# Kernel tuning notes

Measured on AMD Instinct MI355X. Metric: run time of the kernel, lower is better.

Reference implementation:

```python
import jax, jax.numpy as jnp
import numpy as np

N = 50000
IN_C, HID_C, CLS_C = 512, 256, 128
E = 800000


def setup_inputs() -> dict:
    key = jax.random.key(0)
    k1, k2, k3, k4, k5, k6 = jax.random.split(key, 6)
    x = jax.random.normal(k1, (N, IN_C), dtype=jnp.float32)
    edge_index = jax.random.randint(k2, (2, E), 0, N, dtype=jnp.int64)
    # GCNConv params (glorot weights, zero bias as in PyG init)
    W1 = jax.random.normal(k3, (IN_C, HID_C), dtype=jnp.float32) * (1.0 / np.sqrt(IN_C))
    b1 = jnp.zeros((HID_C,), dtype=jnp.float32)
    W2 = jax.random.normal(k4, (HID_C, CLS_C), dtype=jnp.float32) * (1.0 / np.sqrt(HID_C))
    b2 = jnp.zeros((CLS_C,), dtype=jnp.float32)
    return {"x": x, "W1": W1, "b1": b1, "W2": W2, "b2": b2, "edge_index": edge_index}


def _norm_edges(edge_index, n):
    # PyG GCNConv: add self-loops, symmetric normalization deg^-1/2
    loops = jnp.arange(n, dtype=edge_index.dtype)
    src = jnp.concatenate([edge_index[0], loops])
    dst = jnp.concatenate([edge_index[1], loops])
    ones = jnp.ones_like(src, dtype=jnp.float32)
    deg = jax.ops.segment_sum(ones, dst, num_segments=n)
    dinv = jnp.where(deg > 0, jax.lax.rsqrt(deg), 0.0)
    norm = dinv[src] * dinv[dst]  # [E+N]
    return src, dst, norm


def _gcn_conv(x, W, b, src, dst, norm, n):
    h = x @ W  # project first (out_channels < in_channels)
    msg = h[src] * norm[:, None]  # gather + scale, [E+N, C]
    out = jax.ops.segment_sum(msg, dst, num_segments=n)  # scatter-add
    return out + b


def reference(x, W1, b1, W2, b2, edge_index):
    n = x.shape[0]
    src, dst, norm = _norm_edges(edge_index, n)
    h = jax.nn.relu(_gcn_conv(x, W1, b1, src, dst, norm, n))
    # dropout p=0.5 is a no-op in eval mode
    out = _gcn_conv(h, W2, b2, src, dst, norm, n)
    return jax.nn.sigmoid(out)
```

## Files before the change

kernel.cpp:

```cpp
#include <hip/hip_runtime.h>

typedef __attribute__((ext_vector_type(8))) short bf16x8;
typedef __attribute__((ext_vector_type(4))) float f32x4;
typedef unsigned short u16;

__device__ __forceinline__ float bf2f(u16 u) {
  union { unsigned int i; float f; } c; c.i = ((unsigned int)u) << 16; return c.f;
}
__device__ __forceinline__ u16 f2bf(float f) {
  union { float f; unsigned int i; } c; c.f = f;
  unsigned int u = c.i;
  unsigned int r = (u + 0x7FFFu + ((u >> 16) & 1u)) >> 16;
  return (u16)r;
}


__global__ void k_init_deg(int* deg, int n) {
  int i = blockIdx.x * 256 + threadIdx.x;
  if (i < n) deg[i] = 1;
}

__global__ void k_count(const int* __restrict__ ei, int* deg, int E) {
  int e = blockIdx.x * 256 + threadIdx.x;
  if (e < E) atomicAdd(&deg[ei[E + e]], 1);
}

__global__ void k_blocksum(const int* __restrict__ deg, int* bsum, int n) {
  __shared__ int s[256];
  int t = threadIdx.x;
  int i = blockIdx.x * 256 + t;
  s[t] = (i < n) ? (deg[i] - 1) : 0;
  __syncthreads();
  for (int o = 128; o > 0; o >>= 1) {
    if (t < o) s[t] += s[t + o];
    __syncthreads();
  }
  if (t == 0) bsum[blockIdx.x] = s[0];
}

__global__ void k_scanb(const int* __restrict__ bsum, int* bofs, int nb) {
  __shared__ int s[256];
  int t = threadIdx.x;
  int v = (t < nb) ? bsum[t] : 0;
  s[t] = v;
  __syncthreads();
  for (int o = 1; o < 256; o <<= 1) {
    int x = (t >= o) ? s[t - o] : 0;
    __syncthreads();
    s[t] += x;
    __syncthreads();
  }
  bofs[t] = s[t] - v;
}

__global__ void k_rowptr(const int* __restrict__ deg, const int* __restrict__ bofs,
                         int* rowptr, int* cursor, float* dinv, int n) {
  __shared__ int s[256];
  int t = threadIdx.x;
  int i = blockIdx.x * 256 + t;
  int d = (i < n) ? deg[i] : 1;
  int v = (i < n) ? (d - 1) : 0;
  s[t] = v;
  __syncthreads();
  for (int o = 1; o < 256; o <<= 1) {
    int x = (t >= o) ? s[t - o] : 0;
    __syncthreads();
    s[t] += x;
    __syncthreads();
  }
  int excl = s[t] - v + bofs[blockIdx.x];
  if (i < n) {
    rowptr[i] = excl;
    cursor[i] = excl;
    dinv[i] = rsqrtf((float)d);
    if (i == n - 1) rowptr[n] = excl + v;
  }
}

__global__ void k_fill(const int* __restrict__ ei, int* cursor, int* col, int E) {
  int e = blockIdx.x * 256 + threadIdx.x;
  if (e >= E) return;
  int s = ei[e];
  int d = ei[E + e];
  int pos = atomicAdd(&cursor[d], 1);
  col[pos] = s;
}

__global__ void k_twt(const float* __restrict__ W, u16* __restrict__ Wt, int K, int N) {
  int i = blockIdx.x * 256 + threadIdx.x;
  if (i >= K * N) return;
  int k = i / N, n = i - k * N;
  Wt[n * K + k] = f2bf(W[i]);
}


template <bool AF32, int K>
__launch_bounds__(256)
__global__ void gemm_kernel(const void* __restrict__ Ap, const u16* __restrict__ Bt,
                            u16* __restrict__ C, int M, int ldc) {
  __shared__ u16 As[128][40];
  __shared__ u16 Bs[128][40];
  const int tid = threadIdx.x;
  const int lane = tid & 63;
  const int wid = tid >> 6;
  const int wr = wid >> 1, wc = wid & 1;
  const long brow = (long)blockIdx.x * 128;
  const long bcol = (long)blockIdx.y * 128;
  const int srow = tid >> 1;
  const int kb = (tid & 1) << 4;

  f32x4 acc[4][4];
#pragma unroll
  for (int i = 0; i < 4; i++)
#pragma unroll
    for (int j = 0; j < 4; j++) acc[i][j] = (f32x4){0.f, 0.f, 0.f, 0.f};

  union Pack { u16 s[16]; uint4 v[2]; };
  Pack pa, pb;
  constexpr int NT = K / 32;

  auto stage = [&](int kt) {
    const long rgA = brow + srow;
    if constexpr (AF32) {
      const float* A = (const float*)Ap;
      if (rgA < M) {
        const float4* p = (const float4*)(A + rgA * (long)K + kt * 32 + kb);
#pragma unroll
        for (int i = 0; i < 4; i++) {
          float4 v = p[i];
          pa.s[4 * i + 0] = f2bf(v.x);
          pa.s[4 * i + 1] = f2bf(v.y);
          pa.s[4 * i + 2] = f2bf(v.z);
          pa.s[4 * i + 3] = f2bf(v.w);
        }
      } else {
#pragma unroll
        for (int i = 0; i < 16; i++) pa.s[i] = 0;
      }
    } else {
      const u16* A = (const u16*)Ap;
      const uint4* p = (const uint4*)(A + rgA * (long)K + kt * 32 + kb);
      pa.v[0] = p[0];
      pa.v[1] = p[1];
    }
    const uint4* q = (const uint4*)(Bt + (bcol + srow) * (long)K + kt * 32 + kb);
    pb.v[0] = q[0];
    pb.v[1] = q[1];
  };

  stage(0);
  for (int kt = 0; kt < NT; ++kt) {
    __syncthreads();
    *(uint4*)&As[srow][kb] = pa.v[0];
    *(uint4*)&As[srow][kb + 8] = pa.v[1];
    *(uint4*)&Bs[srow][kb] = pb.v[0];
    *(uint4*)&Bs[srow][kb + 8] = pb.v[1];
    __syncthreads();
    if (kt + 1 < NT) stage(kt + 1);

    bf16x8 af[4], bf[4];
#pragma unroll
    for (int i = 0; i < 4; i++)
      af[i] = *(const bf16x8*)&As[wr * 64 + i * 16 + (lane & 15)][(lane >> 4) * 8];
#pragma unroll
    for (int j = 0; j < 4; j++)
      bf[j] = *(const bf16x8*)&Bs[wc * 64 + j * 16 + (lane & 15)][(lane >> 4) * 8];
#pragma unroll
    for (int i = 0; i < 4; i++)
#pragma unroll
      for (int j = 0; j < 4; j++)
        acc[i][j] = __builtin_amdgcn_mfma_f32_16x16x32_bf16(af[i], bf[j], acc[i][j], 0, 0, 0);
  }

#pragma unroll
  for (int i = 0; i < 4; i++) {
    const long r0 = brow + wr * 64 + i * 16 + ((lane >> 4) * 4);
#pragma unroll
    for (int j = 0; j < 4; j++) {
      const long cc = bcol + wc * 64 + j * 16 + (lane & 15);
#pragma unroll
      for (int q = 0; q < 4; q++) {
        long r = r0 + q;
        if (r < M) C[r * (long)ldc + cc] = f2bf(acc[i][j][q]);
      }
    }
  }
}


__launch_bounds__(256)
__global__ void agg1(const u16* __restrict__ h0, const int* __restrict__ rowptr,
                     const int* __restrict__ col, const float* __restrict__ dinv,
                     const float* __restrict__ b1, u16* __restrict__ h, int n) {
  const int wid = threadIdx.x >> 6, lane = threadIdx.x & 63;
  const int node = blockIdx.x * 4 + wid;
  if (node >= n) return;
  const float di = dinv[node];
  ushort4 sv = ((const ushort4*)(h0 + (size_t)node * 256))[lane];
  float a0 = di * bf2f(sv.x), a1 = di * bf2f(sv.y), a2 = di * bf2f(sv.z), a3 = di * bf2f(sv.w);
  int e = rowptr[node];
  const int r1 = rowptr[node + 1];
  for (; e + 4 <= r1; e += 4) {
    int s0 = col[e], s1 = col[e + 1], s2 = col[e + 2], s3 = col[e + 3];
    float c0 = dinv[s0], c1 = dinv[s1], c2 = dinv[s2], c3 = dinv[s3];
    ushort4 v0 = ((const ushort4*)(h0 + (size_t)s0 * 256))[lane];
    ushort4 v1 = ((const ushort4*)(h0 + (size_t)s1 * 256))[lane];
    ushort4 v2 = ((const ushort4*)(h0 + (size_t)s2 * 256))[lane];
    ushort4 v3 = ((const ushort4*)(h0 + (size_t)s3 * 256))[lane];
    a0 += c0 * bf2f(v0.x) + c1 * bf2f(v1.x) + c2 * bf2f(v2.x) + c3 * bf2f(v3.x);
    a1 += c0 * bf2f(v0.y) + c1 * bf2f(v1.y) + c2 * bf2f(v2.y) + c3 * bf2f(v3.y);
    a2 += c0 * bf2f(v0.z) + c1 * bf2f(v1.z) + c2 * bf2f(v2.z) + c3 * bf2f(v3.z);
    a3 += c0 * bf2f(v0.w) + c1 * bf2f(v1.w) + c2 * bf2f(v2.w) + c3 * bf2f(v3.w);
  }
  for (; e < r1; ++e) {
    int s = col[e];
    float c = dinv[s];
    ushort4 v = ((const ushort4*)(h0 + (size_t)s * 256))[lane];
    a0 += c * bf2f(v.x); a1 += c * bf2f(v.y); a2 += c * bf2f(v.z); a3 += c * bf2f(v.w);
  }
  float4 bb = ((const float4*)b1)[lane];
  a0 = a0 * di + bb.x; a1 = a1 * di + bb.y; a2 = a2 * di + bb.z; a3 = a3 * di + bb.w;
  a0 = a0 > 0.f ? a0 : 0.f; a1 = a1 > 0.f ? a1 : 0.f;
  a2 = a2 > 0.f ? a2 : 0.f; a3 = a3 > 0.f ? a3 : 0.f;
  ushort4 o; o.x = f2bf(a0); o.y = f2bf(a1); o.z = f2bf(a2); o.w = f2bf(a3);
  ((ushort4*)(h + (size_t)node * 256))[lane] = o;
}

__device__ __forceinline__ float sigmoidf_(float x) { return 1.f / (1.f + __expf(-x)); }

__launch_bounds__(256)
__global__ void agg2(const u16* __restrict__ h2, const int* __restrict__ rowptr,
                     const int* __restrict__ col, const float* __restrict__ dinv,
                     const float* __restrict__ b2, float* __restrict__ out, int n) {
  const int wid = threadIdx.x >> 6, lane = threadIdx.x & 63;
  const int node = blockIdx.x * 4 + wid;
  if (node >= n) return;
  const float di = dinv[node];
  ushort2 sv = ((const ushort2*)(h2 + (size_t)node * 128))[lane];
  float a0 = di * bf2f(sv.x), a1 = di * bf2f(sv.y);
  int e = rowptr[node];
  const int r1 = rowptr[node + 1];
  for (; e + 4 <= r1; e += 4) {
    int s0 = col[e], s1 = col[e + 1], s2 = col[e + 2], s3 = col[e + 3];
    float c0 = dinv[s0], c1 = dinv[s1], c2 = dinv[s2], c3 = dinv[s3];
    ushort2 v0 = ((const ushort2*)(h2 + (size_t)s0 * 128))[lane];
    ushort2 v1 = ((const ushort2*)(h2 + (size_t)s1 * 128))[lane];
    ushort2 v2 = ((const ushort2*)(h2 + (size_t)s2 * 128))[lane];
    ushort2 v3 = ((const ushort2*)(h2 + (size_t)s3 * 128))[lane];
    a0 += c0 * bf2f(v0.x) + c1 * bf2f(v1.x) + c2 * bf2f(v2.x) + c3 * bf2f(v3.x);
    a1 += c0 * bf2f(v0.y) + c1 * bf2f(v1.y) + c2 * bf2f(v2.y) + c3 * bf2f(v3.y);
  }
  for (; e < r1; ++e) {
    int s = col[e];
    float c = dinv[s];
    ushort2 v = ((const ushort2*)(h2 + (size_t)s * 128))[lane];
    a0 += c * bf2f(v.x); a1 += c * bf2f(v.y);
  }
  float2 bb = ((const float2*)b2)[lane];
  float2 o;
  o.x = sigmoidf_(a0 * di + bb.x);
  o.y = sigmoidf_(a1 * di + bb.y);
  ((float2*)(out + (size_t)node * 128))[lane] = o;
}


extern "C" void kernel_launch(void* const* d_in, const int* in_sizes, int n_in,
                              void* d_out, int out_size, void* d_ws, size_t ws_size,
                              hipStream_t stream) {
  const float* x  = (const float*)d_in[0];
  const float* W1 = (const float*)d_in[1];
  const float* b1 = (const float*)d_in[2];
  const float* W2 = (const float*)d_in[3];
  const float* b2 = (const float*)d_in[4];
  const int*   ei = (const int*)d_in[5];

  const int N = in_sizes[0] / 512;
  const int E = in_sizes[5] / 2;
  const int Mpad = (N + 127) & ~127;
  float* outp = (float*)d_out;

  char* w = (char*)d_ws;
  size_t off = 0;
  auto take = [&](size_t bytes) -> void* {
    void* p = w + off;
    off = (off + bytes + 255) & ~(size_t)255;
    return p;
  };
  u16*   h0     = (u16*)take((size_t)Mpad * 256 * 2);
  u16*   hb     = (u16*)take((size_t)Mpad * 256 * 2);
  u16*   h2     = (u16*)take((size_t)Mpad * 128 * 2);
  u16*   W1t    = (u16*)take(256 * 512 * 2);
  u16*   W2t    = (u16*)take(128 * 256 * 2);
  int*   deg    = (int*)take((size_t)N * 4);
  float* dinv   = (float*)take((size_t)N * 4);
  int*   rowptr = (int*)take((size_t)(N + 1) * 4);
  int*   cursor = (int*)take((size_t)N * 4);
  int*   colx   = (int*)take((size_t)E * 4);
  int*   bsum   = (int*)take(256 * 4);
  int*   bofs   = (int*)take(256 * 4);
  (void)ws_size; (void)n_in; (void)out_size;

  const int nb = (N + 255) / 256;
  const int eb = (E + 255) / 256;

  k_init_deg<<<nb, 256, 0, stream>>>(deg, N);
  k_count<<<eb, 256, 0, stream>>>(ei, deg, E);
  k_blocksum<<<nb, 256, 0, stream>>>(deg, bsum, N);
  k_scanb<<<1, 256, 0, stream>>>(bsum, bofs, nb);
  k_rowptr<<<nb, 256, 0, stream>>>(deg, bofs, rowptr, cursor, dinv, N);
  k_fill<<<eb, 256, 0, stream>>>(ei, cursor, colx, E);
  k_twt<<<(512 * 256 + 255) / 256, 256, 0, stream>>>(W1, W1t, 512, 256);
  k_twt<<<(256 * 128 + 255) / 256, 256, 0, stream>>>(W2, W2t, 256, 128);

  dim3 g1(Mpad / 128, 2);
  gemm_kernel<true, 512><<<g1, 256, 0, stream>>>((const void*)x, W1t, h0, N, 256);
  agg1<<<(N + 3) / 4, 256, 0, stream>>>(h0, rowptr, colx, dinv, b1, hb, N);
  dim3 g2(Mpad / 128, 1);
  gemm_kernel<false, 256><<<g2, 256, 0, stream>>>((const void*)hb, W2t, h2, Mpad, 128);
  agg2<<<(N + 3) / 4, 256, 0, stream>>>(h2, rowptr, colx, dinv, b2, outp, N);
}
```

Measured before the change: 302.5 us.

## Use async global-to-LDS loads with double buffering in GEMM; pack edge weights with columns

The GEMM now loads tiles straight from global memory into LDS with global_load_lds, into swizzled double buffers. fp32 inputs stay in LDS as fp32 and are converted to bf16 with packed convert instructions at fragment-read time, which removes the register staging path and one barrier per k-step. Separately, the CSR fill stores a (src, dinv[src]) pair per edge, so the aggregation kernels skip a dependent random dinv load. The cost is twice the LDS for the fp32 A tile, more bytes per edge in the column array, and clamped out-of-range rows instead of zero fill.

```diff
diff --git a/kernel.cpp b/kernel.cpp
--- a/kernel.cpp
+++ b/kernel.cpp
@@ -1,17 +1,25 @@
 #include <hip/hip_runtime.h>
+#include <type_traits>
 
 typedef __attribute__((ext_vector_type(8))) short bf16x8;
 typedef __attribute__((ext_vector_type(4))) float f32x4;
 typedef unsigned short u16;
+typedef unsigned int u32;
+typedef __attribute__((address_space(1))) const u32 gu32;
+typedef __attribute__((address_space(3))) u32 lu32;
 
 __device__ __forceinline__ float bf2f(u16 u) {
-  union { unsigned int i; float f; } c; c.i = ((unsigned int)u) << 16; return c.f;
+  union { u32 i; float f; } c; c.i = ((u32)u) << 16; return c.f;
 }
 __device__ __forceinline__ u16 f2bf(float f) {
-  union { float f; unsigned int i; } c; c.f = f;
-  unsigned int u = c.i;
-  unsigned int r = (u + 0x7FFFu + ((u >> 16) & 1u)) >> 16;
+  union { float f; u32 i; } c; c.f = f;
+  u32 u = c.i;
+  u32 r = (u + 0x7FFFu + ((u >> 16) & 1u)) >> 16;
   return (u16)r;
+}
+
+__device__ __forceinline__ void gld16(const void* g, void* l) {
+  __builtin_amdgcn_global_load_lds((gu32*)g, (lu32*)l, 16, 0, 0);
 }
 
 
@@ -77,13 +85,14 @@
   }
 }
 
-__global__ void k_fill(const int* __restrict__ ei, int* cursor, int* col, int E) {
+__global__ void k_fill(const int* __restrict__ ei, int* cursor,
+                       const float* __restrict__ dinv, int2* colw, int E) {
   int e = blockIdx.x * 256 + threadIdx.x;
   if (e >= E) return;
   int s = ei[e];
   int d = ei[E + e];
   int pos = atomicAdd(&cursor[d], 1);
-  col[pos] = s;
+  colw[pos] = make_int2(s, __float_as_int(dinv[s]));
 }
 
 __global__ void k_twt(const float* __restrict__ W, u16* __restrict__ Wt, int K, int N) {
@@ -98,16 +107,43 @@
 __launch_bounds__(256)
 __global__ void gemm_kernel(const void* __restrict__ Ap, const u16* __restrict__ Bt,
                             u16* __restrict__ C, int M, int ldc) {
-  __shared__ u16 As[128][40];
-  __shared__ u16 Bs[128][40];
+  using AT = typename std::conditional<AF32, float, u16>::type;
+  __shared__ AT As_[2][4096];
+  __shared__ u16 Bs_[2][4096];
+
   const int tid = threadIdx.x;
   const int lane = tid & 63;
   const int wid = tid >> 6;
   const int wr = wid >> 1, wc = wid & 1;
   const long brow = (long)blockIdx.x * 128;
   const long bcol = (long)blockIdx.y * 128;
-  const int srow = tid >> 1;
-  const int kb = (tid & 1) << 4;
+
+  constexpr int NT = K / 32;
+  constexpr int NJA = AF32 ? 4 : 2;
+
+  const AT* agp[NJA];
+  AT* alp[NJA];
+#pragma unroll
+  for (int j = 0; j < NJA; ++j) {
+    int idx = j * 256 + tid;
+    int row, u;
+    if constexpr (AF32) { row = idx >> 3; u = (idx & 7) ^ (row & 7); }
+    else                { row = idx >> 2; u = (idx & 3) ^ (row & 3); }
+    long grow = brow + row;
+    if (grow > (long)M - 1) grow = M - 1;
+    agp[j] = (const AT*)Ap + grow * (long)K + u * (AF32 ? 4 : 8);
+    alp[j] = &As_[0][idx * (AF32 ? 4 : 8)];
+  }
+  const u16* bgp[2];
+  u16* blp[2];
+#pragma unroll
+  for (int j = 0; j < 2; ++j) {
+    int idx = j * 256 + tid;
+    int row = idx >> 2;
+    int u = (idx & 3) ^ (row & 3);
+    bgp[j] = Bt + (bcol + row) * (long)K + u * 8;
+    blp[j] = &Bs_[0][idx * 8];
+  }
 
   f32x4 acc[4][4];
 #pragma unroll
@@ -115,61 +151,53 @@
 #pragma unroll
     for (int j = 0; j < 4; j++) acc[i][j] = (f32x4){0.f, 0.f, 0.f, 0.f};
 
-  union Pack { u16 s[16]; uint4 v[2]; };
-  Pack pa, pb;
-  constexpr int NT = K / 32;
-
-  auto stage = [&](int kt) {
-    const long rgA = brow + srow;
-    if constexpr (AF32) {
-      const float* A = (const float*)Ap;
-      if (rgA < M) {
-        const float4* p = (const float4*)(A + rgA * (long)K + kt * 32 + kb);
-#pragma unroll
-        for (int i = 0; i < 4; i++) {
-          float4 v = p[i];
-          pa.s[4 * i + 0] = f2bf(v.x);
-          pa.s[4 * i + 1] = f2bf(v.y);
-          pa.s[4 * i + 2] = f2bf(v.z);
-          pa.s[4 * i + 3] = f2bf(v.w);
-        }
+  auto stage = [&](int kt, int buf) {
+    const int boff = buf * 4096;
+#pragma unroll
+    for (int j = 0; j < NJA; ++j) gld16(agp[j] + kt * 32, alp[j] + boff);
+#pragma unroll
+    for (int j = 0; j < 2; ++j) gld16(bgp[j] + kt * 32, blp[j] + boff);
+  };
+
+  stage(0, 0);
+  int cur = 0;
+  for (int kt = 0; kt < NT; ++kt) {
+    __syncthreads();
+    if (kt + 1 < NT) stage(kt + 1, cur ^ 1);
+
+    bf16x8 af[4], bfq[4];
+#pragma unroll
+    for (int i = 0; i < 4; i++) {
+      const int row = wr * 64 + i * 16 + (lane & 15);
+      if constexpr (AF32) {
+        const float* bp = (const float*)&As_[cur][0] + row * 32;
+        const int s = row & 7;
+        const int u0 = (lane >> 4) * 2;
+        float4 x0 = *(const float4*)(bp + (u0 ^ s) * 4);
+        float4 x1 = *(const float4*)(bp + ((u0 + 1) ^ s) * 4);
+        union { u32 w[4]; bf16x8 v; } cv;
+        asm("v_cvt_pk_bf16_f32 %0, %1, %2" : "=v"(cv.w[0]) : "v"(x0.x), "v"(x0.y));
+        asm("v_cvt_pk_bf16_f32 %0, %1, %2" : "=v"(cv.w[1]) : "v"(x0.z), "v"(x0.w));
+        asm("v_cvt_pk_bf16_f32 %0, %1, %2" : "=v"(cv.w[2]) : "v"(x1.x), "v"(x1.y));
+        asm("v_cvt_pk_bf16_f32 %0, %1, %2" : "=v"(cv.w[3]) : "v"(x1.z), "v"(x1.w));
+        af[i] = cv.v;
       } else {
-#pragma unroll
-        for (int i = 0; i < 16; i++) pa.s[i] = 0;
+        const int u = (lane >> 4) ^ (row & 3);
+        af[i] = *(const bf16x8*)((const u16*)&As_[cur][0] + row * 32 + u * 8);
       }
-    } else {
-      const u16* A = (const u16*)Ap;
-      const uint4* p = (const uint4*)(A + rgA * (long)K + kt * 32 + kb);
-      pa.v[0] = p[0];
-      pa.v[1] = p[1];
     }
-    const uint4* q = (const uint4*)(Bt + (bcol + srow) * (long)K + kt * 32 + kb);
-    pb.v[0] = q[0];
-    pb.v[1] = q[1];
-  };
-
-  stage(0);
-  for (int kt = 0; kt < NT; ++kt) {
-    __syncthreads();
-    *(uint4*)&As[srow][kb] = pa.v[0];
-    *(uint4*)&As[srow][kb + 8] = pa.v[1];
-    *(uint4*)&Bs[srow][kb] = pb.v[0];
-    *(uint4*)&Bs[srow][kb + 8] = pb.v[1];
-    __syncthreads();
-    if (kt + 1 < NT) stage(kt + 1);
-
-    bf16x8 af[4], bf[4];
+#pragma unroll
+    for (int j = 0; j < 4; j++) {
+      const int row = wc * 64 + j * 16 + (lane & 15);
+      const int u = (lane >> 4) ^ (row & 3);
+      bfq[j] = *(const bf16x8*)(&Bs_[cur][0] + row * 32 + u * 8);
+    }
 #pragma unroll
     for (int i = 0; i < 4; i++)
-      af[i] = *(const bf16x8*)&As[wr * 64 + i * 16 + (lane & 15)][(lane >> 4) * 8];
-#pragma unroll
-    for (int j = 0; j < 4; j++)
-      bf[j] = *(const bf16x8*)&Bs[wc * 64 + j * 16 + (lane & 15)][(lane >> 4) * 8];
-#pragma unroll
-    for (int i = 0; i < 4; i++)
 #pragma unroll
       for (int j = 0; j < 4; j++)
-        acc[i][j] = __builtin_amdgcn_mfma_f32_16x16x32_bf16(af[i], bf[j], acc[i][j], 0, 0, 0);
+        acc[i][j] = __builtin_amdgcn_mfma_f32_16x16x32_bf16(af[i], bfq[j], acc[i][j], 0, 0, 0);
+    cur ^= 1;
   }
 
 #pragma unroll
@@ -190,7 +218,7 @@
 
 __launch_bounds__(256)
 __global__ void agg1(const u16* __restrict__ h0, const int* __restrict__ rowptr,
-                     const int* __restrict__ col, const float* __restrict__ dinv,
+                     const int2* __restrict__ colw, const float* __restrict__ dinv,
                      const float* __restrict__ b1, u16* __restrict__ h, int n) {
   const int wid = threadIdx.x >> 6, lane = threadIdx.x & 63;
   const int node = blockIdx.x * 4 + wid;
@@ -201,22 +229,23 @@
   int e = rowptr[node];
   const int r1 = rowptr[node + 1];
   for (; e + 4 <= r1; e += 4) {
-    int s0 = col[e], s1 = col[e + 1], s2 = col[e + 2], s3 = col[e + 3];
-    float c0 = dinv[s0], c1 = dinv[s1], c2 = dinv[s2], c3 = dinv[s3];
-    ushort4 v0 = ((const ushort4*)(h0 + (size_t)s0 * 256))[lane];
-    ushort4 v1 = ((const ushort4*)(h0 + (size_t)s1 * 256))[lane];
-    ushort4 v2 = ((const ushort4*)(h0 + (size_t)s2 * 256))[lane];
-    ushort4 v3 = ((const ushort4*)(h0 + (size_t)s3 * 256))[lane];
-    a0 += c0 * bf2f(v0.x) + c1 * bf2f(v1.x) + c2 * bf2f(v2.x) + c3 * bf2f(v3.x);
-    a1 += c0 * bf2f(v0.y) + c1 * bf2f(v1.y) + c2 * bf2f(v2.y) + c3 * bf2f(v3.y);
-    a2 += c0 * bf2f(v0.z) + c1 * bf2f(v1.z) + c2 * bf2f(v2.z) + c3 * bf2f(v3.z);
-    a3 += c0 * bf2f(v0.w) + c1 * bf2f(v1.w) + c2 * bf2f(v2.w) + c3 * bf2f(v3.w);
+    int2 c0 = colw[e], c1 = colw[e + 1], c2 = colw[e + 2], c3 = colw[e + 3];
+    float w0 = __int_as_float(c0.y), w1 = __int_as_float(c1.y);
+    float w2 = __int_as_float(c2.y), w3 = __int_as_float(c3.y);
+    ushort4 v0 = ((const ushort4*)(h0 + (size_t)c0.x * 256))[lane];
+    ushort4 v1 = ((const ushort4*)(h0 + (size_t)c1.x * 256))[lane];
+    ushort4 v2 = ((const ushort4*)(h0 + (size_t)c2.x * 256))[lane];
+    ushort4 v3 = ((const ushort4*)(h0 + (size_t)c3.x * 256))[lane];
+    a0 += w0 * bf2f(v0.x) + w1 * bf2f(v1.x) + w2 * bf2f(v2.x) + w3 * bf2f(v3.x);
+    a1 += w0 * bf2f(v0.y) + w1 * bf2f(v1.y) + w2 * bf2f(v2.y) + w3 * bf2f(v3.y);
+    a2 += w0 * bf2f(v0.z) + w1 * bf2f(v1.z) + w2 * bf2f(v2.z) + w3 * bf2f(v3.z);
+    a3 += w0 * bf2f(v0.w) + w1 * bf2f(v1.w) + w2 * bf2f(v2.w) + w3 * bf2f(v3.w);
   }
   for (; e < r1; ++e) {
-    int s = col[e];
-    float c = dinv[s];
-    ushort4 v = ((const ushort4*)(h0 + (size_t)s * 256))[lane];
-    a0 += c * bf2f(v.x); a1 += c * bf2f(v.y); a2 += c * bf2f(v.z); a3 += c * bf2f(v.w);
+    int2 c = colw[e];
+    float wv = __int_as_float(c.y);
+    ushort4 v = ((const ushort4*)(h0 + (size_t)c.x * 256))[lane];
+    a0 += wv * bf2f(v.x); a1 += wv * bf2f(v.y); a2 += wv * bf2f(v.z); a3 += wv * bf2f(v.w);
   }
   float4 bb = ((const float4*)b1)[lane];
   a0 = a0 * di + bb.x; a1 = a1 * di + bb.y; a2 = a2 * di + bb.z; a3 = a3 * di + bb.w;
@@ -230,7 +259,7 @@
 
 __launch_bounds__(256)
 __global__ void agg2(const u16* __restrict__ h2, const int* __restrict__ rowptr,
-                     const int* __restrict__ col, const float* __restrict__ dinv,
+                     const int2* __restrict__ colw, const float* __restrict__ dinv,
                      const float* __restrict__ b2, float* __restrict__ out, int n) {
   const int wid = threadIdx.x >> 6, lane = threadIdx.x & 63;
   const int node = blockIdx.x * 4 + wid;
@@ -241,20 +270,21 @@
   int e = rowptr[node];
   const int r1 = rowptr[node + 1];
   for (; e + 4 <= r1; e += 4) {
-    int s0 = col[e], s1 = col[e + 1], s2 = col[e + 2], s3 = col[e + 3];
-    float c0 = dinv[s0], c1 = dinv[s1], c2 = dinv[s2], c3 = dinv[s3];
-    ushort2 v0 = ((const ushort2*)(h2 + (size_t)s0 * 128))[lane];
-    ushort2 v1 = ((const ushort2*)(h2 + (size_t)s1 * 128))[lane];
-    ushort2 v2 = ((const ushort2*)(h2 + (size_t)s2 * 128))[lane];
-    ushort2 v3 = ((const ushort2*)(h2 + (size_t)s3 * 128))[lane];
-    a0 += c0 * bf2f(v0.x) + c1 * bf2f(v1.x) + c2 * bf2f(v2.x) + c3 * bf2f(v3.x);
-    a1 += c0 * bf2f(v0.y) + c1 * bf2f(v1.y) + c2 * bf2f(v2.y) + c3 * bf2f(v3.y);
+    int2 c0 = colw[e], c1 = colw[e + 1], c2 = colw[e + 2], c3 = colw[e + 3];
+    float w0 = __int_as_float(c0.y), w1 = __int_as_float(c1.y);
+    float w2 = __int_as_float(c2.y), w3 = __int_as_float(c3.y);
+    ushort2 v0 = ((const ushort2*)(h2 + (size_t)c0.x * 128))[lane];
+    ushort2 v1 = ((const ushort2*)(h2 + (size_t)c1.x * 128))[lane];
+    ushort2 v2 = ((const ushort2*)(h2 + (size_t)c2.x * 128))[lane];
+    ushort2 v3 = ((const ushort2*)(h2 + (size_t)c3.x * 128))[lane];
+    a0 += w0 * bf2f(v0.x) + w1 * bf2f(v1.x) + w2 * bf2f(v2.x) + w3 * bf2f(v3.x);
+    a1 += w0 * bf2f(v0.y) + w1 * bf2f(v1.y) + w2 * bf2f(v2.y) + w3 * bf2f(v3.y);
   }
   for (; e < r1; ++e) {
-    int s = col[e];
-    float c = dinv[s];
-    ushort2 v = ((const ushort2*)(h2 + (size_t)s * 128))[lane];
-    a0 += c * bf2f(v.x); a1 += c * bf2f(v.y);
+    int2 c = colw[e];
+    float wv = __int_as_float(c.y);
+    ushort2 v = ((const ushort2*)(h2 + (size_t)c.x * 128))[lane];
+    a0 += wv * bf2f(v.x); a1 += wv * bf2f(v.y);
   }
   float2 bb = ((const float2*)b2)[lane];
   float2 o;
@@ -295,7 +325,7 @@
   float* dinv   = (float*)take((size_t)N * 4);
   int*   rowptr = (int*)take((size_t)(N + 1) * 4);
   int*   cursor = (int*)take((size_t)N * 4);
-  int*   colx   = (int*)take((size_t)E * 4);
+  int2*  colw   = (int2*)take((size_t)E * 8);
   int*   bsum   = (int*)take(256 * 4);
   int*   bofs   = (int*)take(256 * 4);
   (void)ws_size; (void)n_in; (void)out_size;
@@ -308,14 +338,14 @@
   k_blocksum<<<nb, 256, 0, stream>>>(deg, bsum, N);
   k_scanb<<<1, 256, 0, stream>>>(bsum, bofs, nb);
   k_rowptr<<<nb, 256, 0, stream>>>(deg, bofs, rowptr, cursor, dinv, N);
-  k_fill<<<eb, 256, 0, stream>>>(ei, cursor, colx, E);
+  k_fill<<<eb, 256, 0, stream>>>(ei, cursor, dinv, colw, E);
   k_twt<<<(512 * 256 + 255) / 256, 256, 0, stream>>>(W1, W1t, 512, 256);
   k_twt<<<(256 * 128 + 255) / 256, 256, 0, stream>>>(W2, W2t, 256, 128);
 
   dim3 g1(Mpad / 128, 2);
   gemm_kernel<true, 512><<<g1, 256, 0, stream>>>((const void*)x, W1t, h0, N, 256);
-  agg1<<<(N + 3) / 4, 256, 0, stream>>>(h0, rowptr, colx, dinv, b1, hb, N);
+  agg1<<<(N + 3) / 4, 256, 0, stream>>>(h0, rowptr, colw, dinv, b1, hb, N);
   dim3 g2(Mpad / 128, 1);
   gemm_kernel<false, 256><<<g2, 256, 0, stream>>>((const void*)hb, W2t, h2, Mpad, 128);
-  agg2<<<(N + 3) / 4, 256, 0, stream>>>(h2, rowptr, colx, dinv, b2, outp, N);
-}
+  agg2<<<(N + 3) / 4, 256, 0, stream>>>(h2, rowptr, colw, dinv, b2, outp, N);
+}
```

Result: faster. 251.9 us (-16.7%).
